# Performance work log

Hardware: AMD Instinct MI355X
Metric: run time of the kernel (lower is better)

## Reference

```python
import jax, jax.numpy as jnp
import numpy as np

SIGMA_DIS = 3.0   # from init_kwargs
KMAX = 16         # max kernel label value (labels in 0..KMAX, 0 = background)


def setup_inputs() -> dict:
    key = jax.random.key(0)
    k1, k2 = jax.random.split(key)
    pred = jax.random.normal(k1, (16, 4, 640, 640), dtype=jnp.float32)
    labels = jax.random.randint(k2, (16, 640, 640), 0, KMAX + 1, dtype=jnp.int32)
    return {"pred_similarities": pred, "kernel_mask_ndi_labels": labels}


def _loss(pred, labels):
    # pred: (B, C, H, W) float; labels: (B, H, W) int in [0, KMAX]
    B, C = pred.shape[0], pred.shape[1]
    p = pred.reshape(B, C, -1)            # (B, C, P)
    lab = labels.reshape(B, -1)           # (B, P)
    sq = jnp.sum(p * p, axis=1)           # (B, P) per-pixel squared norm over channels

    # Per-segment sum of squared pred values and cardinality (scatter-reduce).
    seg_ss = jax.vmap(lambda s, l: jax.ops.segment_sum(s, l, num_segments=KMAX + 1))(sq, lab)            # (B, K+1)
    card = jax.vmap(lambda l: jax.ops.segment_sum(jnp.ones(l.shape, jnp.float32), l, num_segments=KMAX + 1))(lab)  # (B, K+1)

    # Masks for labels i and j are disjoint, so
    # ||pred*m_i/c_i - pred*m_j/c_j||_F^2 = SS_i/c_i^2 + SS_j/c_j^2 exactly.
    m = jnp.where(card > 0, seg_ss / jnp.square(jnp.maximum(card, 1.0)), 0.0)  # (B, K+1)

    ids = jnp.arange(KMAX + 1)
    pair_ok = (ids[:, None] >= 1) & (ids[None, :] > ids[:, None])               # i>=1, j>i
    valid = pair_ok[None, :, :] & (card[:, :, None] > 0) & (card[:, None, :] > 0)  # (B, K+1, K+1)

    s2 = m[:, :, None] + m[:, None, :]
    d = jnp.sqrt(jnp.where(valid, s2, 1.0))        # safe sqrt for masked-out pairs
    # NB: torch.max(norm, 0)[0] on a 0-dim tensor is the identity (no relu clamp) -> replicate.
    term = jnp.log1p(jnp.square(SIGMA_DIS - d))
    pair_sum = jnp.sum(jnp.where(valid, term, 0.0), axis=(1, 2))  # (B,)

    nk = jnp.max(lab, axis=1)                                      # num_kernels per image
    denom = (nk * (nk - 1)).astype(jnp.float32)
    loss_b = jnp.where(nk > 1, pair_sum / jnp.maximum(denom, 1.0), 0.0)
    return jnp.sum(loss_b)


def reference(pred_similarities, kernel_mask_ndi_labels):
    return _loss(pred_similarities, kernel_mask_ndi_labels)
```

## Files before the change

kernel.cpp:

```cpp
#include <hip/hip_runtime.h>

#define K  16
#define NB 16
#define NP 409600
#define NPV (NP / 4)
#define BX 64
#define SIGMA_DIS 3.0f

__global__ __launch_bounds__(256) void seg_reduce_kernel(
    const float* __restrict__ pred,
    const int*   __restrict__ lab,
    float* __restrict__ partial)
{
    const int tid  = threadIdx.x;
    const int b    = blockIdx.y;
    const int bx   = blockIdx.x;
    const int lane = tid & 63;
    const int wave = tid >> 6;

    float ssb[K];
    int   cnt[K];
#pragma unroll
    for (int k = 0; k < K; ++k) { ssb[k] = 0.0f; cnt[k] = 0; }

    const float4* p0 = (const float4*)(pred + ((size_t)b * 4 + 0) * NP);
    const float4* p1 = (const float4*)(pred + ((size_t)b * 4 + 1) * NP);
    const float4* p2 = (const float4*)(pred + ((size_t)b * 4 + 2) * NP);
    const float4* p3 = (const float4*)(pred + ((size_t)b * 4 + 3) * NP);
    const int4*   lb = (const int4*)(lab + (size_t)b * NP);

    for (int v = bx * 256 + tid; v < NPV; v += BX * 256) {
        float4 a = p0[v];
        float4 c = p1[v];
        float4 d = p2[v];
        float4 e = p3[v];
        int4   l = lb[v];

        float s0 = a.x * a.x + c.x * c.x + d.x * d.x + e.x * e.x;
        float s1 = a.y * a.y + c.y * c.y + d.y * d.y + e.y * e.y;
        float s2 = a.z * a.z + c.z * c.z + d.z * d.z + e.z * e.z;
        float s3 = a.w * a.w + c.w * c.w + d.w * d.w + e.w * e.w;

#pragma unroll
        for (int k = 0; k < K; ++k) {
            const int kk = k + 1;
            bool e0 = (l.x == kk);
            bool e1 = (l.y == kk);
            bool e2 = (l.z == kk);
            bool e3 = (l.w == kk);
            ssb[k] += e0 ? s0 : 0.0f;
            ssb[k] += e1 ? s1 : 0.0f;
            ssb[k] += e2 ? s2 : 0.0f;
            ssb[k] += e3 ? s3 : 0.0f;
            cnt[k] += __popcll(__ballot(e0)) + __popcll(__ballot(e1))
                    + __popcll(__ballot(e2)) + __popcll(__ballot(e3));
        }
    }

    __shared__ float red_ss[128][K + 1];
    __shared__ int   cnt_sh[4][K];

    if (lane == 0) {
#pragma unroll
        for (int k = 0; k < K; ++k) cnt_sh[wave][k] = cnt[k];
    }

    for (int s = 128; s >= 1; s >>= 1) {
        if (tid >= s && tid < 2 * s) {
#pragma unroll
            for (int k = 0; k < K; ++k) red_ss[tid - s][k] = ssb[k];
        }
        __syncthreads();
        if (tid < s) {
#pragma unroll
            for (int k = 0; k < K; ++k) ssb[k] += red_ss[tid][k];
        }
        __syncthreads();
    }

    if (tid == 0) {
        float* dst = partial + (size_t)(b * BX + bx) * 32;
#pragma unroll
        for (int k = 0; k < K; ++k) dst[k] = ssb[k];
#pragma unroll
        for (int k = 0; k < K; ++k)
            dst[16 + k] = (float)(cnt_sh[0][k] + cnt_sh[1][k] + cnt_sh[2][k] + cnt_sh[3][k]);
    }
}

__global__ __launch_bounds__(256) void finalize_kernel(
    const float* __restrict__ partial,
    float* __restrict__ out)
{
    __shared__ float m_sh[NB][K];
    __shared__ float c_sh[NB][K];
    __shared__ float inv_denom[NB];
    __shared__ float red[256];

    const int t = threadIdx.x;

    {
        const int b = t >> 4;
        const int k = t & 15;
        float ss = 0.0f, cc = 0.0f;
        const float* p = partial + (size_t)b * BX * 32 + k;
        for (int bx = 0; bx < BX; ++bx) {
            ss += p[bx * 32];
            cc += p[bx * 32 + 16];
        }
        c_sh[b][k] = cc;
        m_sh[b][k] = (cc > 0.0f) ? ss / (cc * cc) : 0.0f;
    }
    __syncthreads();

    if (t < NB) {
        int nk = 0;
        for (int k = K; k >= 1; --k) {
            if (c_sh[t][k - 1] > 0.0f) { nk = k; break; }
        }
        float denom = (float)(nk * (nk - 1));
        inv_denom[t] = (nk > 1) ? 1.0f / fmaxf(denom, 1.0f) : 0.0f;
    }
    __syncthreads();

    float acc = 0.0f;
    for (int e = t; e < NB * K * K; e += 256) {
        const int b  = e >> 8;
        const int ij = e & 255;
        const int ki = ij >> 4;
        const int kj = ij & 15;
        if (kj > ki && c_sh[b][ki] > 0.0f && c_sh[b][kj] > 0.0f) {
            float s2 = m_sh[b][ki] + m_sh[b][kj];
            float dd = sqrtf(s2);
            float x  = SIGMA_DIS - dd;
            acc += log1pf(x * x) * inv_denom[b];
        }
    }

    red[t] = acc;
    __syncthreads();
    for (int s = 128; s > 0; s >>= 1) {
        if (t < s) red[t] += red[t + s];
        __syncthreads();
    }
    if (t == 0) out[0] = red[0];
}

extern "C" void kernel_launch(void* const* d_in, const int* in_sizes, int n_in,
                              void* d_out, int out_size, void* d_ws, size_t ws_size,
                              hipStream_t stream) {
    const float* pred = (const float*)d_in[0];
    const int*   lab  = (const int*)d_in[1];
    float* out = (float*)d_out;

    float* partial = (float*)d_ws;

    dim3 grid(BX, NB);
    seg_reduce_kernel<<<grid, 256, 0, stream>>>(pred, lab, partial);
    finalize_kernel<<<1, 256, 0, stream>>>(partial, out);
}
```

Baseline: 39.72 us.

## Fuse finalize into reduction kernel via last-block atomic counter and wave shuffles

Merges the segment-reduce and finalize kernels into one launch: each block writes its partials, increments a global atomic counter, and the last block to finish runs the pairwise loss. The shared-memory tree reduction of per-segment sums is replaced by wave-level shuffle-xor reductions plus a small cross-wave combine. Partials are stored in a k-major layout so the finalize step can read them with float4 loads. This removes one kernel launch and its gap, at the cost of a memset for the counter and a serial tail in a single block.

```diff
diff --git a/kernel.cpp b/kernel.cpp
--- a/kernel.cpp
+++ b/kernel.cpp
@@ -1,22 +1,29 @@
 #include <hip/hip_runtime.h>
 
-#define K  16
-#define NB 16
-#define NP 409600
+#define K   16
+#define NB  16
+#define NP  409600
 #define NPV (NP / 4)
-#define BX 64
+#define BX  64
+#define NBLK (NB * BX)
 #define SIGMA_DIS 3.0f
 
-__global__ __launch_bounds__(256) void seg_reduce_kernel(
+__global__ __launch_bounds__(256) void disc_loss_kernel(
     const float* __restrict__ pred,
     const int*   __restrict__ lab,
-    float* __restrict__ partial)
+    float* __restrict__ ws,
+    float* __restrict__ out)
 {
     const int tid  = threadIdx.x;
-    const int b    = blockIdx.y;
-    const int bx   = blockIdx.x;
     const int lane = tid & 63;
     const int wave = tid >> 6;
+    const int blk  = blockIdx.x;
+    const int b    = blk >> 6;
+    const int bx   = blk & 63;
+
+    float* ss_part  = ws + 16;
+    float* cnt_part = ss_part + K * NBLK;
+    unsigned int* counter = (unsigned int*)ws;
 
     float ssb[K];
     int   cnt[K];
@@ -57,93 +64,93 @@
         }
     }
 
-    __shared__ float red_ss[128][K + 1];
+#pragma unroll
+    for (int k = 0; k < K; ++k) {
+#pragma unroll
+        for (int m = 1; m < 64; m <<= 1)
+            ssb[k] += __shfl_xor(ssb[k], m, 64);
+    }
+
+    __shared__ float ss_sh[4][K];
     __shared__ int   cnt_sh[4][K];
-
     if (lane == 0) {
 #pragma unroll
-        for (int k = 0; k < K; ++k) cnt_sh[wave][k] = cnt[k];
+        for (int k = 0; k < K; ++k) { ss_sh[wave][k] = ssb[k]; cnt_sh[wave][k] = cnt[k]; }
     }
+    __syncthreads();
 
-    for (int s = 128; s >= 1; s >>= 1) {
-        if (tid >= s && tid < 2 * s) {
-#pragma unroll
-            for (int k = 0; k < K; ++k) red_ss[tid - s][k] = ssb[k];
-        }
-        __syncthreads();
-        if (tid < s) {
-#pragma unroll
-            for (int k = 0; k < K; ++k) ssb[k] += red_ss[tid][k];
-        }
-        __syncthreads();
+    if (tid < K) {
+        float s = ss_sh[0][tid] + ss_sh[1][tid] + ss_sh[2][tid] + ss_sh[3][tid];
+        float c = (float)(cnt_sh[0][tid] + cnt_sh[1][tid] + cnt_sh[2][tid] + cnt_sh[3][tid]);
+        ss_part [tid * NBLK + blk] = s;
+        cnt_part[tid * NBLK + blk] = c;
     }
+    __syncthreads();
 
+    __shared__ int is_last;
     if (tid == 0) {
-        float* dst = partial + (size_t)(b * BX + bx) * 32;
-#pragma unroll
-        for (int k = 0; k < K; ++k) dst[k] = ssb[k];
-#pragma unroll
-        for (int k = 0; k < K; ++k)
-            dst[16 + k] = (float)(cnt_sh[0][k] + cnt_sh[1][k] + cnt_sh[2][k] + cnt_sh[3][k]);
+        __threadfence();
+        unsigned int old = atomicAdd(counter, 1u);
+        is_last = (old == NBLK - 1) ? 1 : 0;
     }
-}
+    __syncthreads();
+    if (!is_last) return;
+    __threadfence();
 
-__global__ __launch_bounds__(256) void finalize_kernel(
-    const float* __restrict__ partial,
-    float* __restrict__ out)
-{
     __shared__ float m_sh[NB][K];
     __shared__ float c_sh[NB][K];
     __shared__ float inv_denom[NB];
     __shared__ float red[256];
 
-    const int t = threadIdx.x;
-
     {
-        const int b = t >> 4;
-        const int k = t & 15;
+        const int fb = tid >> 4;
+        const int fk = tid & 15;
+        const float4* sp = (const float4*)(ss_part  + fk * NBLK + fb * BX);
+        const float4* cp = (const float4*)(cnt_part + fk * NBLK + fb * BX);
         float ss = 0.0f, cc = 0.0f;
-        const float* p = partial + (size_t)b * BX * 32 + k;
-        for (int bx = 0; bx < BX; ++bx) {
-            ss += p[bx * 32];
-            cc += p[bx * 32 + 16];
+#pragma unroll
+        for (int i = 0; i < BX / 4; ++i) {
+            float4 v = sp[i];
+            float4 w = cp[i];
+            ss += v.x + v.y + v.z + v.w;
+            cc += w.x + w.y + w.z + w.w;
         }
-        c_sh[b][k] = cc;
-        m_sh[b][k] = (cc > 0.0f) ? ss / (cc * cc) : 0.0f;
+        c_sh[fb][fk] = cc;
+        m_sh[fb][fk] = (cc > 0.0f) ? ss / (cc * cc) : 0.0f;
     }
     __syncthreads();
 
-    if (t < NB) {
+    if (tid < NB) {
         int nk = 0;
         for (int k = K; k >= 1; --k) {
-            if (c_sh[t][k - 1] > 0.0f) { nk = k; break; }
+            if (c_sh[tid][k - 1] > 0.0f) { nk = k; break; }
         }
         float denom = (float)(nk * (nk - 1));
-        inv_denom[t] = (nk > 1) ? 1.0f / fmaxf(denom, 1.0f) : 0.0f;
+        inv_denom[tid] = (nk > 1) ? 1.0f / fmaxf(denom, 1.0f) : 0.0f;
     }
     __syncthreads();
 
     float acc = 0.0f;
-    for (int e = t; e < NB * K * K; e += 256) {
-        const int b  = e >> 8;
+    for (int e = tid; e < NB * K * K; e += 256) {
+        const int fb = e >> 8;
         const int ij = e & 255;
         const int ki = ij >> 4;
         const int kj = ij & 15;
-        if (kj > ki && c_sh[b][ki] > 0.0f && c_sh[b][kj] > 0.0f) {
-            float s2 = m_sh[b][ki] + m_sh[b][kj];
+        if (kj > ki && c_sh[fb][ki] > 0.0f && c_sh[fb][kj] > 0.0f) {
+            float s2 = m_sh[fb][ki] + m_sh[fb][kj];
             float dd = sqrtf(s2);
             float x  = SIGMA_DIS - dd;
-            acc += log1pf(x * x) * inv_denom[b];
+            acc += log1pf(x * x) * inv_denom[fb];
         }
     }
 
-    red[t] = acc;
+    red[tid] = acc;
     __syncthreads();
     for (int s = 128; s > 0; s >>= 1) {
-        if (t < s) red[t] += red[t + s];
+        if (tid < s) red[tid] += red[tid + s];
         __syncthreads();
     }
-    if (t == 0) out[0] = red[0];
+    if (tid == 0) out[0] = red[0];
 }
 
 extern "C" void kernel_launch(void* const* d_in, const int* in_sizes, int n_in,
@@ -153,9 +160,6 @@
     const int*   lab  = (const int*)d_in[1];
     float* out = (float*)d_out;
 
-    float* partial = (float*)d_ws;
-
-    dim3 grid(BX, NB);
-    seg_reduce_kernel<<<grid, 256, 0, stream>>>(pred, lab, partial);
-    finalize_kernel<<<1, 256, 0, stream>>>(partial, out);
+    hipMemsetAsync(d_ws, 0, 64, stream);
+    disc_loss_kernel<<<NBLK, 256, 0, stream>>>(pred, lab, (float*)d_ws, out);
 }
```

Result: slower. 71.78 us (+80.7%).
